# Optimization experiments

Measured on AMD Instinct MI355X. Metric: run time of the kernel, lower is better.

The kernel has to match this reference:

```python
import jax
import jax.numpy as jnp
from jax import lax
import numpy as np

# Module constants (from init_kwargs)
SCALE = 2
CIN = 256
COUT = 256
KER = 3
R = 4
CMID = CIN // R
PAD = KER // 2          # ConvTranspose2d padding
OUT_PAD = SCALE - 1     # ConvTranspose2d output_padding

B, H, W = 4, 64, 64
HO, WO = H * SCALE, W * SCALE


def conv_transpose2d(x, w, b, stride, padding, output_padding):
    """PyTorch ConvTranspose2d. x: [B,Cin,H,W], w: [Cin,Cout,k,k] (torch layout)."""
    k = w.shape[2]
    # rot180 + swap in/out channels -> regular conv kernel [Cout,Cin,k,k]
    wr = jnp.transpose(jnp.flip(w, (2, 3)), (1, 0, 2, 3))
    pad = (k - 1 - padding, k - 1 - padding + output_padding)
    y = lax.conv_general_dilated(
        x, wr, window_strides=(1, 1), padding=[pad, pad],
        lhs_dilation=(stride, stride),
        dimension_numbers=('NCHW', 'OIHW', 'NCHW'))
    return y + b[None, :, None, None]


def setup_inputs() -> dict:
    key = jax.random.key(0)
    k1, k2, k3, k4, k5 = jax.random.split(key, 5)
    inx = jax.random.normal(k1, (B, CIN, H, W), dtype=jnp.float32)
    mask = jax.random.bernoulli(k2, 0.5, (B, 1, HO, WO)).astype(jnp.float32)
    inv_mask = 1.0 - mask
    # params, initialized per the module's init scheme
    w_high = 0.001 * jax.random.normal(k3, (CIN, COUT, KER, KER), dtype=jnp.float32)
    b_high = jnp.zeros((COUT,), dtype=jnp.float32)
    std1 = float(np.sqrt(2.0 / (CMID * 1 * 1)))
    w_low1 = std1 * jax.random.normal(k4, (CMID, CIN, 1, 1), dtype=jnp.float32)
    b_low1 = jnp.zeros((CMID,), dtype=jnp.float32)
    w_low2 = 0.001 * jax.random.normal(k5, (CMID, COUT, KER, KER), dtype=jnp.float32)
    b_low2 = jnp.zeros((COUT,), dtype=jnp.float32)
    return {"inx": inx, "mask": mask, "inv_mask": inv_mask,
            "w_high": w_high, "b_high": b_high,
            "w_low1": w_low1, "b_low1": b_low1,
            "w_low2": w_low2, "b_low2": b_low2}


def reference(inx, mask, inv_mask, w_high, b_high, w_low1, b_low1, w_low2, b_low2):
    # high branch: full-rank transposed conv, routed by mask
    x1 = conv_transpose2d(inx, w_high, b_high, SCALE, PAD, OUT_PAD) * mask
    # low branch: 1x1 bottleneck then transposed conv, routed by inv_mask
    x2 = jnp.einsum('bchw,oc->bohw', inx, w_low1[:, :, 0, 0]) + b_low1[None, :, None, None]
    x2 = conv_transpose2d(x2, w_low2, b_low2, SCALE, PAD, OUT_PAD) * inv_mask
    return x1 + x2
```

## Files before the change

kernel.cpp:

```cpp
#include <hip/hip_runtime.h>
#include <cstdint>
#include <cstddef>

#define CIN   256
#define COUT  256
#define CMID  64
#define H     64
#define W     64
#define HO    128
#define WO    128
#define BATCH 4

typedef unsigned short u16;
typedef unsigned int   u32;
typedef __attribute__((ext_vector_type(8))) __bf16 bf16x8;
typedef __attribute__((ext_vector_type(4))) float f32x4;

#define XT_ROW  16640
#define X2_ROW  4160

__device__ __forceinline__ u16 f2bf(float f) {
    u32 u = __builtin_bit_cast(u32, f);
    u += 0x7fffu + ((u >> 16) & 1u);
    return (u16)(u >> 16);
}

__global__ __launch_bounds__(256) void k_prep(const float* __restrict__ inx,
                                              const float* __restrict__ w1,
                                              const float* __restrict__ b1,
                                              const float* __restrict__ wH,
                                              const float* __restrict__ wL,
                                              u16* __restrict__ Xt,
                                              u16* __restrict__ X2t,
                                              u16* __restrict__ WPH,
                                              u16* __restrict__ WPL) {
    __shared__ u16 sX[32 * 64 * 8];
    __shared__ u16 sW1[8 * 4 * 64 * 8];
    const int blk = blockIdx.x;
    const int tid = threadIdx.x;

    if (blk >= BATCH * 65) {
        const int pb = blk - BATCH * 65;
        const int t = pb / 8;
        const int kc = pb % 8;
        const int co = tid;
        #pragma unroll
        for (int q = 0; q < 4; ++q) {
            u16 pk[8];
            #pragma unroll
            for (int j = 0; j < 8; ++j) {
                int ci = kc * 32 + q * 8 + j;
                pk[j] = f2bf(wH[((size_t)ci * COUT + co) * 9 + t]);
            }
            *(uint4*)(WPH + ((((size_t)t * 8 + kc) * 4 + q) * 256 + co) * 8) = *(uint4*)pk;
        }
        if (kc < 2) {
            #pragma unroll
            for (int q = 0; q < 4; ++q) {
                u16 pk[8];
                #pragma unroll
                for (int j = 0; j < 8; ++j) {
                    int cm = kc * 32 + q * 8 + j;
                    pk[j] = f2bf(wL[((size_t)cm * COUT + co) * 9 + t]);
                }
                *(uint4*)(WPL + ((((size_t)t * 2 + kc) * 4 + q) * 256 + co) * 8) = *(uint4*)pk;
            }
        }
        return;
    }

    const int b = blk / 65;
    const int y = blk % 65;
    u16* xrow  = Xt  + (size_t)(b * 65 + y) * XT_ROW;
    u16* x2row = X2t + (size_t)(b * 65 + y) * X2_ROW;
    if (y == H) {
        uint4 z = {0, 0, 0, 0};
        for (int i = tid; i < XT_ROW / 8; i += 256) *(uint4*)(xrow + i * 8) = z;
        for (int i = tid; i < X2_ROW / 8; i += 256) *(uint4*)(x2row + i * 8) = z;
        return;
    }

    #pragma unroll
    for (int i = 0; i < 16; ++i) {
        int lin4 = i * 256 + tid;
        float4 v = ((const float4*)w1)[lin4];
        int lin = lin4 * 4;
        int cm = lin >> 8, ci = lin & 255;
        u16* dp = sW1 + (((size_t)(ci >> 3) * 64 + cm) * 8) + (ci & 7);
        dp[0] = f2bf(v.x); dp[1] = f2bf(v.y); dp[2] = f2bf(v.z); dp[3] = f2bf(v.w);
    }

    const int x = tid & 63, g0 = tid >> 6;
    #pragma unroll
    for (int gg = 0; gg < 8; ++gg) {
        const int s = gg * 4 + g0;
        u16 pk[8];
        #pragma unroll
        for (int j = 0; j < 8; ++j)
            pk[j] = f2bf(inx[(((size_t)b * CIN + s * 8 + j) * H + y) * W + x]);
        uint4 v = *(uint4*)pk;
        *(uint4*)(xrow + ((size_t)s * 65 + x) * 8) = v;
        *(uint4*)(sX   + ((size_t)s * 64 + x) * 8) = v;
    }
    if (tid < 32) {
        uint4 z = {0, 0, 0, 0};
        *(uint4*)(xrow + ((size_t)tid * 65 + 64) * 8) = z;
    }
    if (tid < 8) {
        uint4 z = {0, 0, 0, 0};
        *(uint4*)(x2row + ((size_t)tid * 65 + 64) * 8) = z;
    }
    __syncthreads();

    const int wv = tid >> 6, lane = tid & 63, l15 = lane & 15, q = lane >> 4;
    f32x4 acc[4] = {};
    #pragma unroll
    for (int kc = 0; kc < 8; ++kc) {
        bf16x8 bfr = *(const bf16x8*)(sX + ((size_t)(kc * 4 + q) * 64 + wv * 16 + l15) * 8);
        #pragma unroll
        for (int mi = 0; mi < 4; ++mi) {
            bf16x8 af = *(const bf16x8*)(sW1 + (((size_t)kc * 4 + q) * 64 + mi * 16 + l15) * 8);
            acc[mi] = __builtin_amdgcn_mfma_f32_16x16x32_bf16(af, bfr, acc[mi], 0, 0, 0);
        }
    }
    const int xx = wv * 16 + l15;
    #pragma unroll
    for (int mi = 0; mi < 4; ++mi) {
        const int s = mi * 2 + (q >> 1);
        u16 pk[4];
        #pragma unroll
        for (int r = 0; r < 4; ++r)
            pk[r] = f2bf(acc[mi][r] + b1[mi * 16 + q * 4 + r]);
        *(ushort4*)(x2row + ((size_t)s * 65 + xx) * 8 + (q & 1) * 4) = *(ushort4*)&pk[0];
    }
}

template<int NR>
__device__ __forceinline__ void accum_all(const u16* __restrict__ Xt,
                                          const u16* __restrict__ X2t,
                                          const u16* __restrict__ WPH,
                                          const u16* __restrict__ WPL,
                                          int b, int y0, int rowR, int coLane,
                                          int q, int l15,
                                          const int* __restrict__ selE,
                                          const int* __restrict__ selO,
                                          f32x4 ce[4][4], f32x4 co_[4][4]) {
    const bf16x8 z8 = {};
    #pragma unroll 2
    for (int kc = 0; kc < 8; ++kc) {
        #pragma unroll
        for (int dy = 0; dy < NR; ++dy) {
            const int ky = (NR == 1) ? 1 : (dy ? 0 : 2);
            const u16* bp = Xt + (size_t)(b * 65 + y0 + rowR + dy) * XT_ROW
                               + ((size_t)(kc * 4 + q) * 65 + l15) * 8;
            bf16x8 be[4], bo0[4], bo1[4];
            #pragma unroll
            for (int ni = 0; ni < 4; ++ni) {
                bf16x8 b0 = *(const bf16x8*)(bp + ni * 128);
                bf16x8 b1 = *(const bf16x8*)(bp + ni * 128 + 8);
                be[ni]  = selE[ni] ? b0 : z8;
                bo0[ni] = selO[ni] ? b0 : z8;
                bo1[ni] = selO[ni] ? b1 : z8;
            }
            const u16* ap = WPH + ((((size_t)(ky * 3) * 8 + kc) * 4 + q) * 256 + coLane) * 8;
            #pragma unroll
            for (int mi = 0; mi < 4; ++mi) {
                bf16x8 a = *(const bf16x8*)(ap + 65536 + mi * 128);
                #pragma unroll
                for (int ni = 0; ni < 4; ++ni)
                    ce[mi][ni] = __builtin_amdgcn_mfma_f32_16x16x32_bf16(a, be[ni], ce[mi][ni], 0, 0, 0);
            }
            #pragma unroll
            for (int mi = 0; mi < 4; ++mi) {
                bf16x8 a = *(const bf16x8*)(ap + 131072 + mi * 128);
                #pragma unroll
                for (int ni = 0; ni < 4; ++ni)
                    co_[mi][ni] = __builtin_amdgcn_mfma_f32_16x16x32_bf16(a, bo0[ni], co_[mi][ni], 0, 0, 0);
            }
            #pragma unroll
            for (int mi = 0; mi < 4; ++mi) {
                bf16x8 a = *(const bf16x8*)(ap + mi * 128);
                #pragma unroll
                for (int ni = 0; ni < 4; ++ni)
                    co_[mi][ni] = __builtin_amdgcn_mfma_f32_16x16x32_bf16(a, bo1[ni], co_[mi][ni], 0, 0, 0);
            }
        }
    }
    #pragma unroll
    for (int kc = 0; kc < 2; ++kc) {
        #pragma unroll
        for (int dy = 0; dy < NR; ++dy) {
            const int ky = (NR == 1) ? 1 : (dy ? 0 : 2);
            const u16* bp = X2t + (size_t)(b * 65 + y0 + rowR + dy) * X2_ROW
                                + ((size_t)(kc * 4 + q) * 65 + l15) * 8;
            bf16x8 be[4], bo0[4], bo1[4];
            #pragma unroll
            for (int ni = 0; ni < 4; ++ni) {
                bf16x8 b0 = *(const bf16x8*)(bp + ni * 128);
                bf16x8 b1 = *(const bf16x8*)(bp + ni * 128 + 8);
                be[ni]  = selE[ni] ? z8 : b0;
                bo0[ni] = selO[ni] ? z8 : b0;
                bo1[ni] = selO[ni] ? z8 : b1;
            }
            const u16* ap = WPL + ((((size_t)(ky * 3) * 2 + kc) * 4 + q) * 256 + coLane) * 8;
            #pragma unroll
            for (int mi = 0; mi < 4; ++mi) {
                bf16x8 a = *(const bf16x8*)(ap + 16384 + mi * 128);
                #pragma unroll
                for (int ni = 0; ni < 4; ++ni)
                    ce[mi][ni] = __builtin_amdgcn_mfma_f32_16x16x32_bf16(a, be[ni], ce[mi][ni], 0, 0, 0);
            }
            #pragma unroll
            for (int mi = 0; mi < 4; ++mi) {
                bf16x8 a = *(const bf16x8*)(ap + 32768 + mi * 128);
                #pragma unroll
                for (int ni = 0; ni < 4; ++ni)
                    co_[mi][ni] = __builtin_amdgcn_mfma_f32_16x16x32_bf16(a, bo0[ni], co_[mi][ni], 0, 0, 0);
            }
            #pragma unroll
            for (int mi = 0; mi < 4; ++mi) {
                bf16x8 a = *(const bf16x8*)(ap + mi * 128);
                #pragma unroll
                for (int ni = 0; ni < 4; ++ni)
                    co_[mi][ni] = __builtin_amdgcn_mfma_f32_16x16x32_bf16(a, bo1[ni], co_[mi][ni], 0, 0, 0);
            }
        }
    }
}

__global__ __launch_bounds__(256, 2) void k_main(const u16* __restrict__ Xt,
                                                 const u16* __restrict__ X2t,
                                                 const u16* __restrict__ WPH,
                                                 const u16* __restrict__ WPL,
                                                 const float* __restrict__ bH,
                                                 const float* __restrict__ bL,
                                                 const float* __restrict__ mask,
                                                 float* __restrict__ out) {
    const int blk = blockIdx.x;
    const int coH = blk & 1;
    const int yP  = (blk >> 1) & 31;
    const int b   = (blk >> 6) & 3;
    const int py  = blk >> 8;
    const int y0  = yP * 2;

    const int tid = threadIdx.x;
    const int wid = tid >> 6, lane = tid & 63, l15 = lane & 15, q = lane >> 4;
    const int rowR = wid >> 1, coQ = wid & 1;
    const int oy = 2 * (y0 + rowR) + py;
    const int coLane = coH * 128 + coQ * 64 + l15;

    int selE[4], selO[4];
    const float* mrow = mask + ((size_t)b * HO + oy) * WO;
    #pragma unroll
    for (int ni = 0; ni < 4; ++ni) {
        float2 mm = *(const float2*)(mrow + 2 * (ni * 16 + l15));
        selE[ni] = (mm.x != 0.f);
        selO[ni] = (mm.y != 0.f);
    }

    f32x4 ce[4][4] = {}, co_[4][4] = {};
    if (py == 0)
        accum_all<1>(Xt, X2t, WPH, WPL, b, y0, rowR, coLane, q, l15, selE, selO, ce, co_);
    else
        accum_all<2>(Xt, X2t, WPH, WPL, b, y0, rowR, coLane, q, l15, selE, selO, ce, co_);

    #pragma unroll
    for (int mi = 0; mi < 4; ++mi) {
        const int cob = coH * 128 + coQ * 64 + mi * 16 + q * 4;
        float bh[4], bl[4];
        #pragma unroll
        for (int r = 0; r < 4; ++r) { bh[r] = bH[cob + r]; bl[r] = bL[cob + r]; }
        #pragma unroll
        for (int r = 0; r < 4; ++r) {
            float* orow = out + (((size_t)b * COUT + cob + r) * HO + oy) * WO;
            #pragma unroll
            for (int ni = 0; ni < 4; ++ni) {
                const int x = ni * 16 + l15;
                float2 v;
                v.x = ce[mi][ni][r]  + (selE[ni] ? bh[r] : bl[r]);
                v.y = co_[mi][ni][r] + (selO[ni] ? bh[r] : bl[r]);
                *(float2*)(orow + 2 * x) = v;
            }
        }
    }
}

extern "C" void kernel_launch(void* const* d_in, const int* in_sizes, int n_in,
                              void* d_out, int out_size, void* d_ws, size_t ws_size,
                              hipStream_t stream) {
    const float* inx    = (const float*)d_in[0];
    const float* mask   = (const float*)d_in[1];
    const float* w_high = (const float*)d_in[3];
    const float* b_high = (const float*)d_in[4];
    const float* w_low1 = (const float*)d_in[5];
    const float* b_low1 = (const float*)d_in[6];
    const float* w_low2 = (const float*)d_in[7];
    const float* b_low2 = (const float*)d_in[8];
    float* out = (float*)d_out;

    char* ws = (char*)d_ws;
    u16* Xt  = (u16*)(ws);
    u16* X2t = (u16*)(ws + 8652800);
    u16* WPH = (u16*)(ws + 10816000);
    u16* WPL = (u16*)(ws + 11995648);

    k_prep<<<BATCH * 65 + 72, 256, 0, stream>>>(inx, w_low1, b_low1, w_high, w_low2,
                                                Xt, X2t, WPH, WPL);
    k_main<<<512, 256, 0, stream>>>(Xt, X2t, WPH, WPL, b_high, b_low2, mask, out);
}
```

Baseline: 144.4 us.

## Stage weight and input tiles through double-buffered LDS with async global-to-LDS loads

```diff
diff --git a/kernel.cpp b/kernel.cpp
--- a/kernel.cpp
+++ b/kernel.cpp
@@ -18,6 +18,14 @@
 
 #define XT_ROW  16640
 #define X2_ROW  4160
+
+#define AS1 __attribute__((address_space(1)))
+#define AS3 __attribute__((address_space(3)))
+
+__device__ __forceinline__ void g2l16(const void* g, const void* l) {
+    __builtin_amdgcn_global_load_lds((const AS1 u32*)(uintptr_t)g,
+                                     (AS3 u32*)(u32)(uintptr_t)l, 16, 0, 0);
+}
 
 __device__ __forceinline__ u16 f2bf(float f) {
     u32 u = __builtin_bit_cast(u32, f);
@@ -135,96 +143,90 @@
     }
 }
 
+#define SA_G 1536
+#define SB_G 520
+
 template<int NR>
-__device__ __forceinline__ void accum_all(const u16* __restrict__ Xt,
-                                          const u16* __restrict__ X2t,
-                                          const u16* __restrict__ WPH,
-                                          const u16* __restrict__ WPL,
-                                          int b, int y0, int rowR, int coLane,
-                                          int q, int l15,
-                                          const int* __restrict__ selE,
-                                          const int* __restrict__ selO,
-                                          f32x4 ce[4][4], f32x4 co_[4][4]) {
+struct Step {
+    __device__ static constexpr int count() { return NR * 10; }
+    __device__ static bool hi(int c) { return c < NR * 8; }
+    __device__ static int  kc(int c) { int cc = hi(c) ? c : c - NR * 8; return NR == 1 ? cc : cc >> 1; }
+    __device__ static int  dy(int c) { int cc = hi(c) ? c : c - NR * 8; return NR == 1 ? 0 : (cc & 1); }
+    __device__ static int  ky(int c) { return NR == 1 ? 1 : (dy(c) ? 0 : 2); }
+};
+
+template<int NR>
+__device__ __forceinline__ void stage(int c, u16* sAb, u16* sBb,
+                                      const u16* __restrict__ Xt,
+                                      const u16* __restrict__ X2t,
+                                      const u16* __restrict__ WPH,
+                                      const u16* __restrict__ WPL,
+                                      int b, int y0, int coH, int wid, int lane) {
+    const bool hi = Step<NR>::hi(c);
+    const int kc = Step<NR>::kc(c);
+    const int dy = Step<NR>::dy(c);
+    const int ky = Step<NR>::ky(c);
+    const int kcn = hi ? 8 : 2;
+    const u16* Wp = hi ? WPH : WPL;
+    const u16* Xp = hi ? Xt : X2t;
+    const size_t rowStr = hi ? XT_ROW : X2_ROW;
+    #pragma unroll
+    for (int i = 0; i < 6; ++i) {
+        const int seg = i * 4 + wid;
+        const int kx = seg >> 3, qq = (seg >> 1) & 3, h = seg & 1;
+        const u16* src = Wp + ((((size_t)(ky * 3 + kx) * kcn + kc) * 4 + qq) * 256
+                                + coH * 128 + h * 64 + lane) * 8;
+        g2l16(src, sAb + ((size_t)((kx * 4 + qq) * 128 + h * 64)) * 8);
+    }
+    #pragma unroll
+    for (int i = 0; i < 2; ++i) {
+        const u16* src = Xp + (size_t)(b * 65 + y0 + dy + i) * rowStr
+                            + ((size_t)(kc * 4 + wid) * 65 + lane) * 8;
+        g2l16(src, sBb + ((size_t)(i * 4 + wid) * 65) * 8);
+    }
+}
+
+template<int NR>
+__device__ __forceinline__ void compute(int c, const u16* sAb, const u16* sBb,
+                                        int rowR, int coQ, int q, int l15,
+                                        const int* __restrict__ selE,
+                                        const int* __restrict__ selO,
+                                        f32x4 ce[4][4], f32x4 co_[4][4]) {
+    const bool hi = Step<NR>::hi(c);
     const bf16x8 z8 = {};
-    #pragma unroll 2
-    for (int kc = 0; kc < 8; ++kc) {
-        #pragma unroll
-        for (int dy = 0; dy < NR; ++dy) {
-            const int ky = (NR == 1) ? 1 : (dy ? 0 : 2);
-            const u16* bp = Xt + (size_t)(b * 65 + y0 + rowR + dy) * XT_ROW
-                               + ((size_t)(kc * 4 + q) * 65 + l15) * 8;
-            bf16x8 be[4], bo0[4], bo1[4];
-            #pragma unroll
-            for (int ni = 0; ni < 4; ++ni) {
-                bf16x8 b0 = *(const bf16x8*)(bp + ni * 128);
-                bf16x8 b1 = *(const bf16x8*)(bp + ni * 128 + 8);
-                be[ni]  = selE[ni] ? b0 : z8;
-                bo0[ni] = selO[ni] ? b0 : z8;
-                bo1[ni] = selO[ni] ? b1 : z8;
-            }
-            const u16* ap = WPH + ((((size_t)(ky * 3) * 8 + kc) * 4 + q) * 256 + coLane) * 8;
-            #pragma unroll
-            for (int mi = 0; mi < 4; ++mi) {
-                bf16x8 a = *(const bf16x8*)(ap + 65536 + mi * 128);
-                #pragma unroll
-                for (int ni = 0; ni < 4; ++ni)
-                    ce[mi][ni] = __builtin_amdgcn_mfma_f32_16x16x32_bf16(a, be[ni], ce[mi][ni], 0, 0, 0);
-            }
-            #pragma unroll
-            for (int mi = 0; mi < 4; ++mi) {
-                bf16x8 a = *(const bf16x8*)(ap + 131072 + mi * 128);
-                #pragma unroll
-                for (int ni = 0; ni < 4; ++ni)
-                    co_[mi][ni] = __builtin_amdgcn_mfma_f32_16x16x32_bf16(a, bo0[ni], co_[mi][ni], 0, 0, 0);
-            }
-            #pragma unroll
-            for (int mi = 0; mi < 4; ++mi) {
-                bf16x8 a = *(const bf16x8*)(ap + mi * 128);
-                #pragma unroll
-                for (int ni = 0; ni < 4; ++ni)
-                    co_[mi][ni] = __builtin_amdgcn_mfma_f32_16x16x32_bf16(a, bo1[ni], co_[mi][ni], 0, 0, 0);
-            }
-        }
-    }
-    #pragma unroll
-    for (int kc = 0; kc < 2; ++kc) {
-        #pragma unroll
-        for (int dy = 0; dy < NR; ++dy) {
-            const int ky = (NR == 1) ? 1 : (dy ? 0 : 2);
-            const u16* bp = X2t + (size_t)(b * 65 + y0 + rowR + dy) * X2_ROW
-                                + ((size_t)(kc * 4 + q) * 65 + l15) * 8;
-            bf16x8 be[4], bo0[4], bo1[4];
-            #pragma unroll
-            for (int ni = 0; ni < 4; ++ni) {
-                bf16x8 b0 = *(const bf16x8*)(bp + ni * 128);
-                bf16x8 b1 = *(const bf16x8*)(bp + ni * 128 + 8);
-                be[ni]  = selE[ni] ? z8 : b0;
-                bo0[ni] = selO[ni] ? z8 : b0;
-                bo1[ni] = selO[ni] ? z8 : b1;
-            }
-            const u16* ap = WPL + ((((size_t)(ky * 3) * 2 + kc) * 4 + q) * 256 + coLane) * 8;
-            #pragma unroll
-            for (int mi = 0; mi < 4; ++mi) {
-                bf16x8 a = *(const bf16x8*)(ap + 16384 + mi * 128);
-                #pragma unroll
-                for (int ni = 0; ni < 4; ++ni)
-                    ce[mi][ni] = __builtin_amdgcn_mfma_f32_16x16x32_bf16(a, be[ni], ce[mi][ni], 0, 0, 0);
-            }
-            #pragma unroll
-            for (int mi = 0; mi < 4; ++mi) {
-                bf16x8 a = *(const bf16x8*)(ap + 32768 + mi * 128);
-                #pragma unroll
-                for (int ni = 0; ni < 4; ++ni)
-                    co_[mi][ni] = __builtin_amdgcn_mfma_f32_16x16x32_bf16(a, bo0[ni], co_[mi][ni], 0, 0, 0);
-            }
-            #pragma unroll
-            for (int mi = 0; mi < 4; ++mi) {
-                bf16x8 a = *(const bf16x8*)(ap + mi * 128);
-                #pragma unroll
-                for (int ni = 0; ni < 4; ++ni)
-                    co_[mi][ni] = __builtin_amdgcn_mfma_f32_16x16x32_bf16(a, bo1[ni], co_[mi][ni], 0, 0, 0);
-            }
-        }
+    const u16* bp = sBb + (((size_t)(rowR * 4 + q)) * 65 + l15) * 8;
+    bf16x8 be[4], bo0[4], bo1[4];
+    #pragma unroll
+    for (int ni = 0; ni < 4; ++ni) {
+        bf16x8 b0 = *(const bf16x8*)(bp + ni * 128);
+        bf16x8 b1 = *(const bf16x8*)(bp + ni * 128 + 8);
+        const bool kE = hi ? (selE[ni] != 0) : (selE[ni] == 0);
+        const bool kO = hi ? (selO[ni] != 0) : (selO[ni] == 0);
+        be[ni]  = kE ? b0 : z8;
+        bo0[ni] = kO ? b0 : z8;
+        bo1[ni] = kO ? b1 : z8;
+    }
+    const u16* ap = sAb + ((size_t)(q * 128 + coQ * 64 + l15)) * 8;
+    #pragma unroll
+    for (int mi = 0; mi < 4; ++mi) {
+        bf16x8 a = *(const bf16x8*)(ap + (1 * 512 + mi * 16) * 8);
+        #pragma unroll
+        for (int ni = 0; ni < 4; ++ni)
+            ce[mi][ni] = __builtin_amdgcn_mfma_f32_16x16x32_bf16(a, be[ni], ce[mi][ni], 0, 0, 0);
+    }
+    #pragma unroll
+    for (int mi = 0; mi < 4; ++mi) {
+        bf16x8 a = *(const bf16x8*)(ap + (2 * 512 + mi * 16) * 8);
+        #pragma unroll
+        for (int ni = 0; ni < 4; ++ni)
+            co_[mi][ni] = __builtin_amdgcn_mfma_f32_16x16x32_bf16(a, bo0[ni], co_[mi][ni], 0, 0, 0);
+    }
+    #pragma unroll
+    for (int mi = 0; mi < 4; ++mi) {
+        bf16x8 a = *(const bf16x8*)(ap + (mi * 16) * 8);
+        #pragma unroll
+        for (int ni = 0; ni < 4; ++ni)
+            co_[mi][ni] = __builtin_amdgcn_mfma_f32_16x16x32_bf16(a, bo1[ni], co_[mi][ni], 0, 0, 0);
     }
 }
 
@@ -236,6 +238,9 @@
                                                  const float* __restrict__ bL,
                                                  const float* __restrict__ mask,
                                                  float* __restrict__ out) {
+    __shared__ u16 sA[2][SA_G * 8];
+    __shared__ u16 sB[2][SB_G * 8];
+
     const int blk = blockIdx.x;
     const int coH = blk & 1;
     const int yP  = (blk >> 1) & 31;
@@ -247,7 +252,6 @@
     const int wid = tid >> 6, lane = tid & 63, l15 = lane & 15, q = lane >> 4;
     const int rowR = wid >> 1, coQ = wid & 1;
     const int oy = 2 * (y0 + rowR) + py;
-    const int coLane = coH * 128 + coQ * 64 + l15;
 
     int selE[4], selO[4];
     const float* mrow = mask + ((size_t)b * HO + oy) * WO;
@@ -258,11 +262,38 @@
         selO[ni] = (mm.y != 0.f);
     }
 
+    if (tid < 16) {
+        uint4 z = {0, 0, 0, 0};
+        *(uint4*)(sB[tid >> 3] + (((size_t)(tid & 7)) * 65 + 64) * 8) = z;
+    }
+
     f32x4 ce[4][4] = {}, co_[4][4] = {};
-    if (py == 0)
-        accum_all<1>(Xt, X2t, WPH, WPL, b, y0, rowR, coLane, q, l15, selE, selO, ce, co_);
-    else
-        accum_all<2>(Xt, X2t, WPH, WPL, b, y0, rowR, coLane, q, l15, selE, selO, ce, co_);
+
+    if (py == 0) {
+        constexpr int NS = Step<1>::count();
+        stage<1>(0, sA[0], sB[0], Xt, X2t, WPH, WPL, b, y0, coH, wid, lane);
+        __syncthreads();
+        #pragma unroll
+        for (int c = 0; c < NS; ++c) {
+            if (c + 1 < NS)
+                stage<1>(c + 1, sA[(c + 1) & 1], sB[(c + 1) & 1],
+                         Xt, X2t, WPH, WPL, b, y0, coH, wid, lane);
+            compute<1>(c, sA[c & 1], sB[c & 1], rowR, coQ, q, l15, selE, selO, ce, co_);
+            __syncthreads();
+        }
+    } else {
+        constexpr int NS = Step<2>::count();
+        stage<2>(0, sA[0], sB[0], Xt, X2t, WPH, WPL, b, y0, coH, wid, lane);
+        __syncthreads();
+        #pragma unroll
+        for (int c = 0; c < NS; ++c) {
+            if (c + 1 < NS)
+                stage<2>(c + 1, sA[(c + 1) & 1], sB[(c + 1) & 1],
+                         Xt, X2t, WPH, WPL, b, y0, coH, wid, lane);
+            compute<2>(c, sA[c & 1], sB[c & 1], rowR, coQ, q, l15, selE, selO, ce, co_);
+            __syncthreads();
+        }
+    }
 
     #pragma unroll
     for (int mi = 0; mi < 4; ++mi) {
```

New measurement: 125.7 us. -13.0%, faster.
